# Performance work log

Measured on AMD Instinct MI355X. Metric: run time of the kernel, lower is better.

The kernel has to match this reference:

```python
import jax, jax.numpy as jnp
import numpy as np

B, T, IN, H = 4096, 100, 140, 256


def setup_inputs() -> dict:
    key = jax.random.key(0)
    ks = jax.random.split(key, 13)
    s = 1.0 / np.sqrt(H)  # PyTorch LSTM/Linear default init scale
    u = lambda k, shape: jax.random.uniform(k, shape, jnp.float32, -s, s)
    return {
        "x": jax.random.normal(ks[0], (B, T, IN), jnp.float32),
        # LSTM layer 0 (input 140 -> hidden 256), PyTorch gate order i,f,g,o
        "W_ih0": u(ks[1], (4 * H, IN)),
        "W_hh0": u(ks[2], (4 * H, H)),
        "b_ih0": u(ks[3], (4 * H,)),
        "b_hh0": u(ks[4], (4 * H,)),
        # LSTM layer 1 (hidden 256 -> hidden 256)
        "W_ih1": u(ks[5], (4 * H, H)),
        "W_hh1": u(ks[6], (4 * H, H)),
        "b_ih1": u(ks[7], (4 * H,)),
        "b_hh1": u(ks[8], (4 * H,)),
        # advantage MLP: Linear(256,256) -> ReLU -> Linear(256,1)
        "W_a1": u(ks[9], (H, H)),
        "b_a1": u(ks[10], (H,)),
        "W_a2": u(ks[11], (1, H)),
        "b_a2": u(ks[12], (1,)),
    }


def _lstm_cell(xt, h, c, W_ih, W_hh, b):
    # xt: (B, in), h/c: (B, H). PyTorch gate order: i, f, g, o.
    g = xt @ W_ih.T + h @ W_hh.T + b
    i, f, gg, o = jnp.split(g, 4, axis=-1)
    c_new = jax.nn.sigmoid(f) * c + jax.nn.sigmoid(i) * jnp.tanh(gg)
    h_new = jax.nn.sigmoid(o) * jnp.tanh(c_new)
    return h_new, c_new


def reference(x, W_ih0, W_hh0, b_ih0, b_hh0, W_ih1, W_hh1, b_ih1, b_hh1,
              W_a1, b_a1, W_a2, b_a2):
    Bx = x.shape[0]
    b0 = b_ih0 + b_hh0
    b1 = b_ih1 + b_hh1

    def step(carry, xt):
        h0, c0, h1, c1 = carry
        h0, c0 = _lstm_cell(xt, h0, c0, W_ih0, W_hh0, b0)
        h1, c1 = _lstm_cell(h0, h1, c1, W_ih1, W_hh1, b1)
        a = jax.nn.relu(h1 @ W_a1.T + b_a1) @ W_a2.T + b_a2  # (B, 1)
        return (h0, c0, h1, c1), a[:, 0]

    init = tuple(jnp.zeros((Bx, H), x.dtype) for _ in range(4))
    _, outs = jax.lax.scan(step, init, jnp.swapaxes(x, 0, 1))  # (T, B)
    # Faithful to torch.cat(outputs).view(B, -1): flatten in t-major order,
    # then reshape to (B, T) (this scrambles batch/time exactly as the original).
    return outs.reshape(Bx, -1)
```

## Files before the change

kernel.cpp:

```cpp
#include <hip/hip_runtime.h>
#include <cstdint>
#include <cstddef>

#define T_STEPS 100
#define IN_DIM  140
#define HDIM    256
#define BTOT    4096
#define MROWS   16
#define NBLK    (BTOT/MROWS)
#define NTHR    512

typedef _Float16 f16;
typedef _Float16 f16x8 __attribute__((ext_vector_type(8)));
typedef float    f32x4 __attribute__((ext_vector_type(4)));

#define NS0 13
#define NS1 16
#define NSA 8
#define E0 (NS0*64*512)
#define E1 (NS1*64*512)
#define EA (NSA*16*512)
#define F16TOT (E0+E1+EA)
#define EB 2048
#define PREP_TOT (F16TOT+EB)

#define ACOLS 680
#define H0COL 160
#define H1COL 416

__device__ __forceinline__ float sigmoidf_(float x) {
    return 1.0f / (1.0f + __expf(-x));
}
__device__ __forceinline__ float tanhf_(float x) {
    return 1.0f - 2.0f / (__expf(2.0f * x) + 1.0f);
}

__global__ void prep(const float* __restrict__ Wih0, const float* __restrict__ Whh0,
                     const float* __restrict__ bih0, const float* __restrict__ bhh0,
                     const float* __restrict__ Wih1, const float* __restrict__ Whh1,
                     const float* __restrict__ bih1, const float* __restrict__ bhh1,
                     const float* __restrict__ Wa1,  f16* __restrict__ wsf,
                     float* __restrict__ wsb)
{
    int idx = blockIdx.x * 256 + threadIdx.x;
    if (idx < E0) {
        int e = idx & 7, l = (idx >> 3) & 63, fi = idx >> 9;
        int nt = fi & 63, ks = fi >> 6;
        int k = ks * 32 + ((l >> 4) << 3) + e;
        int n = nt * 16 + (l & 15);
        float v = (k < 160) ? (k < IN_DIM ? Wih0[n * IN_DIM + k] : 0.f)
                            : Whh0[n * HDIM + (k - 160)];
        wsf[idx] = (f16)v;
    } else if (idx < E0 + E1) {
        int i2 = idx - E0;
        int e = i2 & 7, l = (i2 >> 3) & 63, fi = i2 >> 9;
        int nt = fi & 63, ks = fi >> 6;
        int k = ks * 32 + ((l >> 4) << 3) + e;
        int n = nt * 16 + (l & 15);
        float v = (k < HDIM) ? Wih1[n * HDIM + k] : Whh1[n * HDIM + (k - HDIM)];
        wsf[idx] = (f16)v;
    } else if (idx < F16TOT) {
        int i3 = idx - (E0 + E1);
        int e = i3 & 7, l = (i3 >> 3) & 63, fi = i3 >> 9;
        int nt = fi & 15, ks = fi >> 4;
        int k = ks * 32 + ((l >> 4) << 3) + e;
        int j = nt * 16 + (l & 15);
        wsf[idx] = (f16)Wa1[j * HDIM + k];
    } else if (idx < PREP_TOT) {
        int i4 = idx - F16TOT;
        if (i4 < 1024) wsb[i4] = bih0[i4] + bhh0[i4];
        else           wsb[i4] = bih1[i4 - 1024] + bhh1[i4 - 1024];
    }
}

#define GLOAD_LDS(gsrc, ldst)                                              \
    __builtin_amdgcn_global_load_lds(                                      \
        (const __attribute__((address_space(1))) void*)(gsrc),             \
        (__attribute__((address_space(3))) void*)(ldst), 16, 0, 0)

__device__ __forceinline__ void stage8(const f16* slice, f16* dst, int w, int l) {
    #pragma unroll
    for (int g = 0; g < 4; g++)
        #pragma unroll
        for (int q = 0; q < 2; q++) {
            const f16* src = slice + (size_t)(g * 16 + 2 * w + q) * 512 + l * 8;
            GLOAD_LDS(src, dst + (g * 2 + q) * 512);
        }
}

template<int N>
__device__ __forceinline__ void wait_vm() {
    asm volatile("s_waitcnt vmcnt(%0)" :: "i"(N) : "memory");
    __builtin_amdgcn_sched_barrier(0);
}
#define WAIT_LGKM0 do { asm volatile("s_waitcnt lgkmcnt(0)" ::: "memory"); \
                        __builtin_amdgcn_sched_barrier(0); } while (0)
#define BAR_LG do { asm volatile("s_waitcnt lgkmcnt(0)" ::: "memory");     \
                    __builtin_amdgcn_sched_barrier(0);                     \
                    __builtin_amdgcn_s_barrier();                          \
                    __builtin_amdgcn_sched_barrier(0); } while (0)

__global__ __launch_bounds__(NTHR) void lstm_mfma(
    const float* __restrict__ x, const f16* __restrict__ wsf,
    const float* __restrict__ wsb, const float* __restrict__ Wa2,
    const float* __restrict__ ba1, const float* __restrict__ ba2,
    float* __restrict__ out)
{
    __shared__ __align__(16) f16 A[MROWS][ACOLS];
    __shared__ __align__(16) f16 Bst[8][2][4096];
    __shared__ float red[8][MROWS];

    const int tid = threadIdx.x;
    const int l   = tid & 63;
    const int w   = tid >> 6;
    const int lm  = l & 15;
    const int lk  = (l >> 4) << 3;
    const int m0  = (l >> 4) << 2;
    const int row0 = blockIdx.x * MROWS;

    const f16* W0 = wsf;
    const f16* W1 = wsf + E0;
    const f16* WA = wsf + E0 + E1;
    f16* wbuf = &Bst[w][0][0];

    for (int i = tid; i < MROWS * ACOLS; i += NTHR) ((f16*)A)[i] = (f16)0.f;

    const int u0 = (2 * w) * 16 + lm;
    const int u1 = (2 * w + 1) * 16 + lm;
    float b0v[2][4], b1v[2][4];
    #pragma unroll
    for (int g = 0; g < 4; g++) {
        b0v[0][g] = wsb[g * 256 + u0];          b0v[1][g] = wsb[g * 256 + u1];
        b1v[0][g] = wsb[1024 + g * 256 + u0];   b1v[1][g] = wsb[1024 + g * 256 + u1];
    }
    const float bAv[2]  = { ba1[u0], ba1[u1] };
    const float wa2v[2] = { Wa2[u0], Wa2[u1] };
    const float ba2v    = ba2[0];

    f16x8 advw[16];
    #pragma unroll
    for (int ks = 0; ks < NSA; ks++) {
        advw[2 * ks + 0] = *(const f16x8*)(WA + (size_t)(ks * 16 + 2 * w + 0) * 512 + l * 8);
        advw[2 * ks + 1] = *(const f16x8*)(WA + (size_t)(ks * 16 + 2 * w + 1) * 512 + l * 8);
    }

    float c0s[2][4], c1s[2][4];
    #pragma unroll
    for (int q = 0; q < 2; q++)
        #pragma unroll
        for (int r = 0; r < 4; r++) { c0s[q][r] = 0.f; c1s[q][r] = 0.f; }

    __syncthreads();

    for (int i = tid; i < MROWS * IN_DIM; i += NTHR) {
        int b = i / IN_DIM, k = i - b * IN_DIM;
        A[b][k] = (f16)x[(size_t)(row0 + b) * (T_STEPS * IN_DIM) + k];
    }
    stage8(W0, wbuf, w, l);
    __syncthreads();

    #pragma unroll 1
    for (int t = 0; t < T_STEPS; t++) {
        const int p = t & 1;

        f32x4 acc[2][4];
        #pragma unroll
        for (int q = 0; q < 2; q++)
            #pragma unroll
            for (int g = 0; g < 4; g++) {
                float b = b0v[q][g];
                acc[q][g] = (f32x4){b, b, b, b};
            }
        #pragma unroll 1
        for (int ks = 0; ks < NS0; ks++) {
            WAIT_LGKM0;
            {
                f16* db = wbuf + (((ks + 1 + p) & 1) << 12);
                if (ks < NS0 - 1) stage8(W0 + (size_t)(ks + 1) * 64 * 512, db, w, l);
                else              stage8(W1, db, w, l);
            }
            wait_vm<8>();
            const f16* rb = wbuf + (((ks + p) & 1) << 12);
            f16x8 a0 = *(const f16x8*)&A[lm][ks * 32 + lk];
            #pragma unroll
            for (int g = 0; g < 4; g++)
                #pragma unroll
                for (int q = 0; q < 2; q++) {
                    f16x8 bf = *(const f16x8*)(rb + (g * 2 + q) * 512 + l * 8);
                    acc[q][g] = __builtin_amdgcn_mfma_f32_16x16x32_f16(a0, bf, acc[q][g], 0, 0, 0);
                }
        }

        f16 hnew[2][4];
        #pragma unroll
        for (int q = 0; q < 2; q++)
            #pragma unroll
            for (int r = 0; r < 4; r++) {
                float ig = sigmoidf_(acc[q][0][r]);
                float fg = sigmoidf_(acc[q][1][r]);
                float gv = tanhf_   (acc[q][2][r]);
                float og = sigmoidf_(acc[q][3][r]);
                float c  = fmaf(fg, c0s[q][r], ig * gv);
                c0s[q][r] = c;
                hnew[q][r] = (f16)(og * tanhf_(c));
            }
        BAR_LG;
        #pragma unroll
        for (int r = 0; r < 4; r++) {
            A[m0 + r][H0COL + u0] = hnew[0][r];
            A[m0 + r][H0COL + u1] = hnew[1][r];
        }
        BAR_LG;

        #pragma unroll
        for (int q = 0; q < 2; q++)
            #pragma unroll
            for (int g = 0; g < 4; g++) {
                float b = b1v[q][g];
                acc[q][g] = (f32x4){b, b, b, b};
            }
        #pragma unroll 1
        for (int ks = 0; ks < NS1; ks++) {
            WAIT_LGKM0;
            {
                f16* db = wbuf + (((ks + p) & 1) << 12);
                if (ks < NS1 - 1) stage8(W1 + (size_t)(ks + 1) * 64 * 512, db, w, l);
                else              stage8(W0, db, w, l);
            }
            wait_vm<8>();
            const f16* rb = wbuf + (((ks + 1 + p) & 1) << 12);
            f16x8 a0 = *(const f16x8*)&A[lm][H0COL + ks * 32 + lk];
            #pragma unroll
            for (int g = 0; g < 4; g++)
                #pragma unroll
                for (int q = 0; q < 2; q++) {
                    f16x8 bf = *(const f16x8*)(rb + (g * 2 + q) * 512 + l * 8);
                    acc[q][g] = __builtin_amdgcn_mfma_f32_16x16x32_f16(a0, bf, acc[q][g], 0, 0, 0);
                }
        }

        #pragma unroll
        for (int q = 0; q < 2; q++)
            #pragma unroll
            for (int r = 0; r < 4; r++) {
                float ig = sigmoidf_(acc[q][0][r]);
                float fg = sigmoidf_(acc[q][1][r]);
                float gv = tanhf_   (acc[q][2][r]);
                float og = sigmoidf_(acc[q][3][r]);
                float c  = fmaf(fg, c1s[q][r], ig * gv);
                c1s[q][r] = c;
                hnew[q][r] = (f16)(og * tanhf_(c));
            }
        BAR_LG;
        #pragma unroll
        for (int r = 0; r < 4; r++) {
            A[m0 + r][H1COL + u0] = hnew[0][r];
            A[m0 + r][H1COL + u1] = hnew[1][r];
        }
        BAR_LG;

        f32x4 accA[2];
        #pragma unroll
        for (int q = 0; q < 2; q++) {
            float b = bAv[q];
            accA[q] = (f32x4){b, b, b, b};
        }
        #pragma unroll
        for (int ks = 0; ks < NSA; ks++) {
            f16x8 a0 = *(const f16x8*)&A[lm][H1COL + ks * 32 + lk];
            accA[0] = __builtin_amdgcn_mfma_f32_16x16x32_f16(a0, advw[2 * ks + 0], accA[0], 0, 0, 0);
            accA[1] = __builtin_amdgcn_mfma_f32_16x16x32_f16(a0, advw[2 * ks + 1], accA[1], 0, 0, 0);
        }

        {
            const int tn = (t + 1 < T_STEPS) ? (t + 1) : t;
            for (int i = tid; i < MROWS * IN_DIM; i += NTHR) {
                int b = i / IN_DIM, k = i - b * IN_DIM;
                A[b][k] = (f16)x[(size_t)(row0 + b) * (T_STEPS * IN_DIM) + (size_t)tn * IN_DIM + k];
            }
        }

        float s[4];
        #pragma unroll
        for (int r = 0; r < 4; r++)
            s[r] = fmaxf(accA[0][r], 0.f) * wa2v[0] + fmaxf(accA[1][r], 0.f) * wa2v[1];
        #pragma unroll
        for (int msk = 1; msk < 16; msk <<= 1)
            #pragma unroll
            for (int r = 0; r < 4; r++)
                s[r] += __shfl_xor(s[r], msk, 64);
        if (lm == 0) {
            #pragma unroll
            for (int r = 0; r < 4; r++) red[w][m0 + r] = s[r];
        }
        BAR_LG;
        if (tid < MROWS) {
            float o = ba2v;
            #pragma unroll
            for (int w2 = 0; w2 < 8; w2++) o += red[w2][tid];
            out[(size_t)t * BTOT + row0 + tid] = o;
        }
    }
}

extern "C" void kernel_launch(void* const* d_in, const int* in_sizes, int n_in,
                              void* d_out, int out_size, void* d_ws, size_t ws_size,
                              hipStream_t stream)
{
    const float* x    = (const float*)d_in[0];
    const float* Wih0 = (const float*)d_in[1];
    const float* Whh0 = (const float*)d_in[2];
    const float* bih0 = (const float*)d_in[3];
    const float* bhh0 = (const float*)d_in[4];
    const float* Wih1 = (const float*)d_in[5];
    const float* Whh1 = (const float*)d_in[6];
    const float* bih1 = (const float*)d_in[7];
    const float* bhh1 = (const float*)d_in[8];
    const float* Wa1  = (const float*)d_in[9];
    const float* ba1  = (const float*)d_in[10];
    const float* Wa2  = (const float*)d_in[11];
    const float* ba2  = (const float*)d_in[12];

    f16*   wsf = (f16*)d_ws;
    float* wsb = (float*)((char*)d_ws + (size_t)F16TOT * sizeof(f16));
    float* out = (float*)d_out;

    hipLaunchKernelGGL(prep, dim3(PREP_TOT / 256), dim3(256), 0, stream,
                       Wih0, Whh0, bih0, bhh0, Wih1, Whh1, bih1, bhh1, Wa1, wsf, wsb);
    hipLaunchKernelGGL(lstm_mfma, dim3(NBLK), dim3(NTHR), 0, stream,
                       x, wsf, wsb, Wa2, ba1, ba2, out);
}
```

Measured before the change: 2.162 ms.

## Stream LSTM weights directly into registers instead of LDS double-buffering

Replaces the per-wave LDS double buffer for recurrent weights (global_load_lds plus waitcnt choreography) with direct global-to-register loads of the next k-slice, prefetched one step ahead in a cur/nxt register pair. The advantage-MLP weights move from 16 persistent VGPR fragments into LDS so registers are available for the prefetch buffers. This removes LDS write/read traffic and explicit waits on the weight path, but depends on the compiler scheduling global load latency behind the MFMAs and raises register pressure.

```diff
diff --git a/kernel.cpp b/kernel.cpp
--- a/kernel.cpp
+++ b/kernel.cpp
@@ -78,27 +78,14 @@
         (const __attribute__((address_space(1))) void*)(gsrc),             \
         (__attribute__((address_space(3))) void*)(ldst), 16, 0, 0)
 
-__device__ __forceinline__ void stage8(const f16* slice, f16* dst, int w, int l) {
-    #pragma unroll
-    for (int g = 0; g < 4; g++)
-        #pragma unroll
-        for (int q = 0; q < 2; q++) {
-            const f16* src = slice + (size_t)(g * 16 + 2 * w + q) * 512 + l * 8;
-            GLOAD_LDS(src, dst + (g * 2 + q) * 512);
-        }
-}
-
-template<int N>
-__device__ __forceinline__ void wait_vm() {
-    asm volatile("s_waitcnt vmcnt(%0)" :: "i"(N) : "memory");
-    __builtin_amdgcn_sched_barrier(0);
-}
-#define WAIT_LGKM0 do { asm volatile("s_waitcnt lgkmcnt(0)" ::: "memory"); \
-                        __builtin_amdgcn_sched_barrier(0); } while (0)
 #define BAR_LG do { asm volatile("s_waitcnt lgkmcnt(0)" ::: "memory");     \
                     __builtin_amdgcn_sched_barrier(0);                     \
                     __builtin_amdgcn_s_barrier();                          \
                     __builtin_amdgcn_sched_barrier(0); } while (0)
+
+__device__ __forceinline__ f16x8 ldfrag(const f16* base, int f, int w, int l) {
+    return *(const f16x8*)(base + ((size_t)(((f >> 1) << 4) + 2 * w + (f & 1)) << 9) + l * 8);
+}
 
 __global__ __launch_bounds__(NTHR) void lstm_mfma(
     const float* __restrict__ x, const f16* __restrict__ wsf,
@@ -107,7 +94,7 @@
     float* __restrict__ out)
 {
     __shared__ __align__(16) f16 A[MROWS][ACOLS];
-    __shared__ __align__(16) f16 Bst[8][2][4096];
+    __shared__ __align__(16) f16 advL[8 * 16 * 512];
     __shared__ float red[8][MROWS];
 
     const int tid = threadIdx.x;
@@ -121,7 +108,6 @@
     const f16* W0 = wsf;
     const f16* W1 = wsf + E0;
     const f16* WA = wsf + E0 + E1;
-    f16* wbuf = &Bst[w][0][0];
 
     for (int i = tid; i < MROWS * ACOLS; i += NTHR) ((f16*)A)[i] = (f16)0.f;
 
@@ -137,11 +123,10 @@
     const float wa2v[2] = { Wa2[u0], Wa2[u1] };
     const float ba2v    = ba2[0];
 
-    f16x8 advw[16];
     #pragma unroll
-    for (int ks = 0; ks < NSA; ks++) {
-        advw[2 * ks + 0] = *(const f16x8*)(WA + (size_t)(ks * 16 + 2 * w + 0) * 512 + l * 8);
-        advw[2 * ks + 1] = *(const f16x8*)(WA + (size_t)(ks * 16 + 2 * w + 1) * 512 + l * 8);
+    for (int fi = 0; fi < 16; fi++) {
+        const f16* src = WA + ((size_t)(((fi >> 1) << 4) + 2 * w + (fi & 1)) << 9) + l * 8;
+        GLOAD_LDS(src, advL + (size_t)(w * 16 + fi) * 512);
     }
 
     float c0s[2][4], c1s[2][4];
@@ -150,19 +135,18 @@
         #pragma unroll
         for (int r = 0; r < 4; r++) { c0s[q][r] = 0.f; c1s[q][r] = 0.f; }
 
-    __syncthreads();
-
     for (int i = tid; i < MROWS * IN_DIM; i += NTHR) {
         int b = i / IN_DIM, k = i - b * IN_DIM;
         A[b][k] = (f16)x[(size_t)(row0 + b) * (T_STEPS * IN_DIM) + k];
     }
-    stage8(W0, wbuf, w, l);
+    f16x8 cur[8];
+    #pragma unroll
+    for (int f = 0; f < 8; f++) cur[f] = ldfrag(W0, f, w, l);
+
     __syncthreads();
 
     #pragma unroll 1
     for (int t = 0; t < T_STEPS; t++) {
-        const int p = t & 1;
-
         f32x4 acc[2][4];
         #pragma unroll
         for (int q = 0; q < 2; q++)
@@ -173,22 +157,18 @@
             }
         #pragma unroll 1
         for (int ks = 0; ks < NS0; ks++) {
-            WAIT_LGKM0;
-            {
-                f16* db = wbuf + (((ks + 1 + p) & 1) << 12);
-                if (ks < NS0 - 1) stage8(W0 + (size_t)(ks + 1) * 64 * 512, db, w, l);
-                else              stage8(W1, db, w, l);
-            }
-            wait_vm<8>();
-            const f16* rb = wbuf + (((ks + p) & 1) << 12);
+            const f16* nb = (ks < NS0 - 1) ? (W0 + (size_t)(ks + 1) * (64 * 512)) : W1;
+            f16x8 nxt[8];
+            #pragma unroll
+            for (int f = 0; f < 8; f++) nxt[f] = ldfrag(nb, f, w, l);
             f16x8 a0 = *(const f16x8*)&A[lm][ks * 32 + lk];
             #pragma unroll
             for (int g = 0; g < 4; g++)
                 #pragma unroll
-                for (int q = 0; q < 2; q++) {
-                    f16x8 bf = *(const f16x8*)(rb + (g * 2 + q) * 512 + l * 8);
-                    acc[q][g] = __builtin_amdgcn_mfma_f32_16x16x32_f16(a0, bf, acc[q][g], 0, 0, 0);
-                }
+                for (int q = 0; q < 2; q++)
+                    acc[q][g] = __builtin_amdgcn_mfma_f32_16x16x32_f16(a0, cur[g * 2 + q], acc[q][g], 0, 0, 0);
+            #pragma unroll
+            for (int f = 0; f < 8; f++) cur[f] = nxt[f];
         }
 
         f16 hnew[2][4];
@@ -221,22 +201,18 @@
             }
         #pragma unroll 1
         for (int ks = 0; ks < NS1; ks++) {
-            WAIT_LGKM0;
-            {
-                f16* db = wbuf + (((ks + p) & 1) << 12);
-                if (ks < NS1 - 1) stage8(W1 + (size_t)(ks + 1) * 64 * 512, db, w, l);
-                else              stage8(W0, db, w, l);
-            }
-            wait_vm<8>();
-            const f16* rb = wbuf + (((ks + 1 + p) & 1) << 12);
+            const f16* nb = (ks < NS1 - 1) ? (W1 + (size_t)(ks + 1) * (64 * 512)) : W0;
+            f16x8 nxt[8];
+            #pragma unroll
+            for (int f = 0; f < 8; f++) nxt[f] = ldfrag(nb, f, w, l);
             f16x8 a0 = *(const f16x8*)&A[lm][H0COL + ks * 32 + lk];
             #pragma unroll
             for (int g = 0; g < 4; g++)
                 #pragma unroll
-                for (int q = 0; q < 2; q++) {
-                    f16x8 bf = *(const f16x8*)(rb + (g * 2 + q) * 512 + l * 8);
-                    acc[q][g] = __builtin_amdgcn_mfma_f32_16x16x32_f16(a0, bf, acc[q][g], 0, 0, 0);
-                }
+                for (int q = 0; q < 2; q++)
+                    acc[q][g] = __builtin_amdgcn_mfma_f32_16x16x32_f16(a0, cur[g * 2 + q], acc[q][g], 0, 0, 0);
+            #pragma unroll
+            for (int f = 0; f < 8; f++) cur[f] = nxt[f];
         }
 
         #pragma unroll
@@ -268,8 +244,10 @@
         #pragma unroll
         for (int ks = 0; ks < NSA; ks++) {
             f16x8 a0 = *(const f16x8*)&A[lm][H1COL + ks * 32 + lk];
-            accA[0] = __builtin_amdgcn_mfma_f32_16x16x32_f16(a0, advw[2 * ks + 0], accA[0], 0, 0, 0);
-            accA[1] = __builtin_amdgcn_mfma_f32_16x16x32_f16(a0, advw[2 * ks + 1], accA[1], 0, 0, 0);
+            f16x8 bf0 = *(const f16x8*)(advL + (size_t)(w * 16 + 2 * ks + 0) * 512 + l * 8);
+            f16x8 bf1 = *(const f16x8*)(advL + (size_t)(w * 16 + 2 * ks + 1) * 512 + l * 8);
+            accA[0] = __builtin_amdgcn_mfma_f32_16x16x32_f16(a0, bf0, accA[0], 0, 0, 0);
+            accA[1] = __builtin_amdgcn_mfma_f32_16x16x32_f16(a0, bf1, accA[1], 0, 0, 0);
         }
 
         {
```

Result: faster. 1.998 ms (-7.6%).
